# Kernel optimization log

Hardware: AMD Instinct MI355X
Metric: run time of the kernel (lower is better)

Reference implementation:

```python
import jax, jax.numpy as jnp
import numpy as np
from jax.scipy.special import logsumexp

B, N, D, H = 8, 2048, 3, 256
BLUR = 0.001            # geomloss blur
EPS0 = 32.0             # ~diameter^2/2 for unit-std gaussian clouds
N_ITERS = 14            # eps-scaling steps down to blur^2
EPS_LIST = np.geomspace(EPS0, BLUR ** 2, N_ITERS).astype(np.float32)


def _sqdist(x, y):
    # x: [B,N,3], y: [B,M,3] -> [B,N,M] squared euclidean distance
    x2 = jnp.sum(x * x, -1)[:, :, None]
    y2 = jnp.sum(y * y, -1)[:, None, :]
    xy = jnp.einsum('bnd,bmd->bnm', x, y)
    return jnp.maximum(x2 + y2 - 2.0 * xy, 0.0)


def sinkhorn_potential_g(x, y):
    """Log-domain Sinkhorn (p=2 cost ||x-y||^2/2, uniform weights) with
    epsilon scaling; returns second dual potential g over y. Mimics
    geomloss.SamplesLoss('sinkhorn', p=2, blur=0.001, potentials=True)."""
    C = 0.5 * _sqdist(x, y)                      # [B,N,M]
    n, m = x.shape[1], y.shape[1]
    loga = -jnp.log(jnp.float32(n))
    logb = -jnp.log(jnp.float32(m))
    f = jnp.zeros((x.shape[0], n), C.dtype)
    g = jnp.zeros((x.shape[0], m), C.dtype)
    for eps in EPS_LIST:
        f = -eps * logsumexp(logb + (g[:, None, :] - C) / eps, axis=2)
        g = -eps * logsumexp(loga + (f[:, :, None] - C) / eps, axis=1)
    return g


def get_hard_assignment(x, y):
    # idx such that y[idx] is the OT match for x
    g = sinkhorn_potential_g(x, y)                       # [B,M]
    C_minus_g = _sqdist(x, y) - g[:, None, :]            # [B,N,M]
    return jnp.argmin(C_minus_g, axis=2)                 # [B,N]


def setup_inputs() -> dict:
    key = jax.random.key(0)
    ks = jax.random.split(key, 8)
    return {
        'cloud': jax.random.normal(ks[0], (B, N, D), jnp.float32),
        'noise': jax.random.normal(ks[1], (B, N, D), jnp.float32),
        't': jax.random.uniform(ks[2], (B,), jnp.float32),
        'W1': jax.random.normal(ks[3], (D, H), jnp.float32) * 0.1,
        'Wt': jax.random.normal(ks[4], (H,), jnp.float32) * 0.1,
        'b1': jnp.zeros((H,), jnp.float32),
        'W2': jax.random.normal(ks[5], (H, D), jnp.float32) * 0.1,
        'b2': jnp.zeros((D,), jnp.float32),
    }


def reference(cloud, noise, t, W1, Wt, b1, W2, b2):
    # std normalization (torch.std -> unbiased, ddof=1), done under no_grad
    std = jnp.std(cloud, axis=(1, 2), keepdims=True, ddof=1)
    x0 = cloud / std
    idx = get_hard_assignment(noise, x0)                 # [B,N] int
    x0_aligned = jnp.take_along_axis(x0, idx[:, :, None], axis=1)  # [B,N,3]
    tv = t[:, None, None]
    x_t = (1.0 - tv) * x0_aligned + tv * noise
    # stand-in diffusion network: per-point MLP conditioned on t
    h = jax.nn.relu(jnp.einsum('bnd,dh->bnh', x_t, W1) + tv * Wt + b1)
    v_pred = jnp.einsum('bnh,hd->bnd', h, W2) + b2
    v = noise - x0_aligned
    return v_pred, v
```

## Files before the change

### kernel.cpp

```cpp
#include <hip/hip_runtime.h>
#include <math.h>

#define B_ 8
#define N_ 2048
#define D_ 3
#define H_ 256
#define ND_ (N_*D_)
#define BN_ (B_*N_)

__global__ __launch_bounds__(256) void stdprep_kernel(const float* __restrict__ cloud,
    const float* __restrict__ noise,
    float4* __restrict__ x0p, float4* __restrict__ np4,
    float* __restrict__ f, float* __restrict__ g) {
  __shared__ float red[256];
  int b = blockIdx.x, tid = threadIdx.x;
  const float* p = cloud + (size_t)b * ND_;
  float s = 0.f;
  for (int i = tid; i < ND_; i += 256) s += p[i];
  red[tid] = s; __syncthreads();
  for (int off = 128; off > 0; off >>= 1) {
    if (tid < off) red[tid] += red[tid + off];
    __syncthreads();
  }
  float mean = red[0] / (float)ND_;
  __syncthreads();
  float ss = 0.f;
  for (int i = tid; i < ND_; i += 256) { float d = p[i] - mean; ss += d * d; }
  red[tid] = ss; __syncthreads();
  for (int off = 128; off > 0; off >>= 1) {
    if (tid < off) red[tid] += red[tid + off];
    __syncthreads();
  }
  float sd = sqrtf(red[0] / (float)(ND_ - 1));
  int base = b * N_;
  for (int i = tid; i < N_; i += 256) {
    int gi = base + i;
    float cx = cloud[3*gi] / sd, cy = cloud[3*gi+1] / sd, cz = cloud[3*gi+2] / sd;
    x0p[gi] = make_float4(cx, cy, cz, cx*cx + cy*cy + cz*cz);
    float ax = noise[3*gi], ay = noise[3*gi+1], az = noise[3*gi+2];
    np4[gi] = make_float4(ax, ay, az, ax*ax + ay*ay + az*az);
    f[gi] = 0.f; g[gi] = 0.f;
  }
}

__global__ __launch_bounds__(512, 4) void lse_kernel(
    const float4* __restrict__ outer, const float4* __restrict__ inner,
    const float* __restrict__ pin, float* __restrict__ pout,
    float scl, float kk, float hh, float c1, float c2) {
  __shared__ float4 sP[N_];
  int tid = threadIdx.x;
  int b = blockIdx.x & 7;
  int rowBase = (blockIdx.x >> 3) << 4;
  int base = b * N_;
  for (int j = tid; j < N_; j += 512) {
    float4 p = inner[base + j];
    float q = kk * pin[base + j] - hh * p.w;
    sP[j] = make_float4(scl * p.x, scl * p.y, scl * p.z, q);
  }
  __syncthreads();
  int wave = tid >> 6, lane = tid & 63;
  int r0 = base + rowBase + (wave << 1);
  float4 A0 = outer[r0], A1 = outer[r0+1];
  float a0x = scl*A0.x, a0y = scl*A0.y, a0z = scl*A0.z, rc0 = -hh*A0.w;
  float a1x = scl*A1.x, a1y = scl*A1.y, a1z = scl*A1.z, rc1 = -hh*A1.w;
  float v0[32], v1[32];
  float m0 = -INFINITY, m1 = -INFINITY;
#pragma unroll
  for (int jj = 0; jj < 32; ++jj) {
    float4 p = sP[(jj << 6) + lane];
    float t0 = fmaf(p.x, a0x, p.w); t0 = fmaf(p.y, a0y, t0); t0 = fmaf(p.z, a0z, t0);
    v0[jj] = t0; m0 = fmaxf(m0, t0);
    float t1 = fmaf(p.x, a1x, p.w); t1 = fmaf(p.y, a1y, t1); t1 = fmaf(p.z, a1z, t1);
    v1[jj] = t1; m1 = fmaxf(m1, t1);
  }
#pragma unroll
  for (int off = 32; off >= 1; off >>= 1) {
    m0 = fmaxf(m0, __shfl_xor(m0, off, 64));
    m1 = fmaxf(m1, __shfl_xor(m1, off, 64));
  }
  float s0 = 0.f, s1 = 0.f;
#pragma unroll
  for (int jj = 0; jj < 32; ++jj) {
    s0 += __builtin_amdgcn_exp2f(v0[jj] - m0);
    s1 += __builtin_amdgcn_exp2f(v1[jj] - m1);
  }
#pragma unroll
  for (int off = 32; off >= 1; off >>= 1) {
    s0 += __shfl_xor(s0, off, 64);
    s1 += __shfl_xor(s1, off, 64);
  }
  if (lane == 0) {
    pout[r0]   = fmaf(c1, rc0 + m0 + __builtin_amdgcn_logf(s0), c2);
    pout[r0+1] = fmaf(c1, rc1 + m1 + __builtin_amdgcn_logf(s1), c2);
  }
}

__global__ __launch_bounds__(256) void assign_mlp_kernel(
    const float4* __restrict__ np4, const float4* __restrict__ x0p,
    const float* __restrict__ g, const float* __restrict__ t,
    const float* __restrict__ W1, const float* __restrict__ Wt,
    const float* __restrict__ b1, const float* __restrict__ W2,
    const float* __restrict__ b2, float* __restrict__ out) {
  __shared__ float4 sPts[N_];
  __shared__ float  sg[N_];
  __shared__ float  sW1[3*H_], sWt[H_], sb1[H_], sW2[H_*3], sb2[3];
  int tid = threadIdx.x;
  int b = blockIdx.x & 7;
  int rowBase = (blockIdx.x >> 3) << 4;
  int base = b * N_;
  for (int j = tid; j < N_; j += 256) { sPts[j] = x0p[base+j]; sg[j] = g[base+j]; }
  for (int i = tid; i < 3*H_; i += 256) { sW1[i] = W1[i]; sW2[i] = W2[i]; }
  if (tid < H_) { sWt[tid] = Wt[tid]; sb1[tid] = b1[tid]; }
  if (tid < 3) sb2[tid] = b2[tid];
  __syncthreads();
  int wave = tid >> 6, lane = tid & 63;
  int r0 = base + rowBase + (wave << 2);
  float4 A0 = np4[r0], A1 = np4[r0+1], A2 = np4[r0+2], A3 = np4[r0+3];
  float b0 = INFINITY, b1v = INFINITY, b2v = INFINITY, b3v = INFINITY;
  int i0 = 0, i1 = 0, i2 = 0, i3 = 0;
#pragma unroll
  for (int jj = 0; jj < 32; ++jj) {
    int j = (jj << 6) + lane;
    float4 p = sPts[j];
    float gj = sg[j];
    float d0 = A0.x*p.x + A0.y*p.y + A0.z*p.z;
    float v0 = fmaxf(A0.w + p.w - 2.0f*d0, 0.0f) - gj;
    if (v0 < b0) { b0 = v0; i0 = j; }
    float d1 = A1.x*p.x + A1.y*p.y + A1.z*p.z;
    float v1 = fmaxf(A1.w + p.w - 2.0f*d1, 0.0f) - gj;
    if (v1 < b1v) { b1v = v1; i1 = j; }
    float d2 = A2.x*p.x + A2.y*p.y + A2.z*p.z;
    float v2 = fmaxf(A2.w + p.w - 2.0f*d2, 0.0f) - gj;
    if (v2 < b2v) { b2v = v2; i2 = j; }
    float d3 = A3.x*p.x + A3.y*p.y + A3.z*p.z;
    float v3 = fmaxf(A3.w + p.w - 2.0f*d3, 0.0f) - gj;
    if (v3 < b3v) { b3v = v3; i3 = j; }
  }
#pragma unroll
  for (int off = 32; off >= 1; off >>= 1) {
    float ov; int oi;
    ov = __shfl_xor(b0, off, 64);  oi = __shfl_xor(i0, off, 64);
    if (ov < b0 || (ov == b0 && oi < i0)) { b0 = ov; i0 = oi; }
    ov = __shfl_xor(b1v, off, 64); oi = __shfl_xor(i1, off, 64);
    if (ov < b1v || (ov == b1v && oi < i1)) { b1v = ov; i1 = oi; }
    ov = __shfl_xor(b2v, off, 64); oi = __shfl_xor(i2, off, 64);
    if (ov < b2v || (ov == b2v && oi < i2)) { b2v = ov; i2 = oi; }
    ov = __shfl_xor(b3v, off, 64); oi = __shfl_xor(i3, off, 64);
    if (ov < b3v || (ov == b3v && oi < i3)) { b3v = ov; i3 = oi; }
  }
  float tb = t[b];
  int idx[4] = {i0, i1, i2, i3};
  float4 Ar[4] = {A0, A1, A2, A3};
#pragma unroll
  for (int rr = 0; rr < 4; ++rr) {
    float4 A = Ar[rr];
    float4 xa = sPts[idx[rr]];
    float xtx = (1.0f - tb)*xa.x + tb*A.x;
    float xty = (1.0f - tb)*xa.y + tb*A.y;
    float xtz = (1.0f - tb)*xa.z + tb*A.z;
    float acc0 = 0.f, acc1 = 0.f, acc2 = 0.f;
#pragma unroll
    for (int hh = 0; hh < 4; ++hh) {
      int h = (hh << 6) + lane;
      float hv = xtx*sW1[h] + xty*sW1[H_+h] + xtz*sW1[2*H_+h] + tb*sWt[h] + sb1[h];
      hv = fmaxf(hv, 0.0f);
      acc0 += hv * sW2[3*h];
      acc1 += hv * sW2[3*h+1];
      acc2 += hv * sW2[3*h+2];
    }
#pragma unroll
    for (int off = 32; off >= 1; off >>= 1) {
      acc0 += __shfl_xor(acc0, off, 64);
      acc1 += __shfl_xor(acc1, off, 64);
      acc2 += __shfl_xor(acc2, off, 64);
    }
    if (lane == 0) {
      int gi = r0 + rr;
      out[3*gi]   = acc0 + sb2[0];
      out[3*gi+1] = acc1 + sb2[1];
      out[3*gi+2] = acc2 + sb2[2];
      out[3*BN_ + 3*gi]   = A.x - xa.x;
      out[3*BN_ + 3*gi+1] = A.y - xa.y;
      out[3*BN_ + 3*gi+2] = A.z - xa.z;
    }
  }
}

extern "C" void kernel_launch(void* const* d_in, const int* in_sizes, int n_in,
                              void* d_out, int out_size, void* d_ws, size_t ws_size,
                              hipStream_t stream) {
  (void)in_sizes; (void)n_in; (void)out_size; (void)ws_size;
  const float* cloud = (const float*)d_in[0];
  const float* noise = (const float*)d_in[1];
  const float* t     = (const float*)d_in[2];
  const float* W1    = (const float*)d_in[3];
  const float* Wt    = (const float*)d_in[4];
  const float* b1    = (const float*)d_in[5];
  const float* W2    = (const float*)d_in[6];
  const float* b2w   = (const float*)d_in[7];
  float* out = (float*)d_out;

  float* ws   = (float*)d_ws;
  float4* x0p = (float4*)(ws + 16);
  float4* np4 = (float4*)(ws + 16 + 4*BN_);
  float* f    = ws + 16 + 8*BN_;
  float* g    = f + BN_;

  stdprep_kernel<<<B_, 256, 0, stream>>>(cloud, noise, x0p, np4, f, g);

  const double LOG2E = 1.4426950408889634074;
  const double LN2   = 0.6931471805599453094;
  const double logw  = -log(2048.0);
  const double l0 = log10(32.0), l1 = log10(1e-6);
  for (int kit = 0; kit < 14; ++kit) {
    double epsd = pow(10.0, l0 + (l1 - l0) * ((double)kit / 13.0));
    float eps = (float)epsd;
    float kk  = (float)(LOG2E / (double)eps);
    float hh  = 0.5f * kk;
    float scl = sqrtf(kk);
    float c1  = (float)(-(double)eps * LN2);
    float c2  = (float)(-(double)eps * logw);
    lse_kernel<<<B_*(N_/16), 512, 0, stream>>>(np4, x0p, g, f, scl, kk, hh, c1, c2);
    lse_kernel<<<B_*(N_/16), 512, 0, stream>>>(x0p, np4, f, g, scl, kk, hh, c1, c2);
  }

  assign_mlp_kernel<<<B_*(N_/16), 256, 0, stream>>>(np4, x0p, g, t, W1, Wt, b1, W2, b2w, out);
}
```

Baseline: 389.0 us.

## Use online one-pass logsumexp with four rows per wave in Sinkhorn LSE

Replaces the two-pass max-then-sum log-sum-exp with an online running max/sum that rescales the accumulator as it goes. This removes the per-thread value arrays, so the launch bound is raised for higher occupancy. Each wave now processes four rows instead of two, halving the block count and the shared-memory staging per row, and outer-row loads are hoisted before the barrier. The trade-off is roughly twice as many exp2 evaluations per element plus a more complex cross-lane merge, which may hurt an exp-bound kernel.

```diff
diff --git a/kernel.cpp b/kernel.cpp
--- a/kernel.cpp
+++ b/kernel.cpp
@@ -43,55 +43,75 @@
   }
 }
 
-__global__ __launch_bounds__(512, 4) void lse_kernel(
+__global__ __launch_bounds__(512, 8) void lse_kernel(
     const float4* __restrict__ outer, const float4* __restrict__ inner,
     const float* __restrict__ pin, float* __restrict__ pout,
     float scl, float kk, float hh, float c1, float c2) {
   __shared__ float4 sP[N_];
   int tid = threadIdx.x;
   int b = blockIdx.x & 7;
-  int rowBase = (blockIdx.x >> 3) << 4;
+  int rowBase = (blockIdx.x >> 3) << 5;
   int base = b * N_;
+  int wave = tid >> 6, lane = tid & 63;
+  int r0 = base + rowBase + (wave << 2);
+  float4 A0 = outer[r0], A1 = outer[r0+1], A2 = outer[r0+2], A3 = outer[r0+3];
   for (int j = tid; j < N_; j += 512) {
     float4 p = inner[base + j];
     float q = kk * pin[base + j] - hh * p.w;
     sP[j] = make_float4(scl * p.x, scl * p.y, scl * p.z, q);
   }
-  __syncthreads();
-  int wave = tid >> 6, lane = tid & 63;
-  int r0 = base + rowBase + (wave << 1);
-  float4 A0 = outer[r0], A1 = outer[r0+1];
   float a0x = scl*A0.x, a0y = scl*A0.y, a0z = scl*A0.z, rc0 = -hh*A0.w;
   float a1x = scl*A1.x, a1y = scl*A1.y, a1z = scl*A1.z, rc1 = -hh*A1.w;
-  float v0[32], v1[32];
-  float m0 = -INFINITY, m1 = -INFINITY;
+  float a2x = scl*A2.x, a2y = scl*A2.y, a2z = scl*A2.z, rc2 = -hh*A2.w;
+  float a3x = scl*A3.x, a3y = scl*A3.y, a3z = scl*A3.z, rc3 = -hh*A3.w;
+  __syncthreads();
+  float m0 = -INFINITY, m1 = -INFINITY, m2 = -INFINITY, m3 = -INFINITY;
+  float s0 = 0.f, s1 = 0.f, s2 = 0.f, s3 = 0.f;
 #pragma unroll
   for (int jj = 0; jj < 32; ++jj) {
     float4 p = sP[(jj << 6) + lane];
     float t0 = fmaf(p.x, a0x, p.w); t0 = fmaf(p.y, a0y, t0); t0 = fmaf(p.z, a0z, t0);
-    v0[jj] = t0; m0 = fmaxf(m0, t0);
+    float n0 = fmaxf(m0, t0);
+    s0 = fmaf(s0, __builtin_amdgcn_exp2f(m0 - n0), __builtin_amdgcn_exp2f(t0 - n0));
+    m0 = n0;
     float t1 = fmaf(p.x, a1x, p.w); t1 = fmaf(p.y, a1y, t1); t1 = fmaf(p.z, a1z, t1);
-    v1[jj] = t1; m1 = fmaxf(m1, t1);
+    float n1 = fmaxf(m1, t1);
+    s1 = fmaf(s1, __builtin_amdgcn_exp2f(m1 - n1), __builtin_amdgcn_exp2f(t1 - n1));
+    m1 = n1;
+    float t2 = fmaf(p.x, a2x, p.w); t2 = fmaf(p.y, a2y, t2); t2 = fmaf(p.z, a2z, t2);
+    float n2 = fmaxf(m2, t2);
+    s2 = fmaf(s2, __builtin_amdgcn_exp2f(m2 - n2), __builtin_amdgcn_exp2f(t2 - n2));
+    m2 = n2;
+    float t3 = fmaf(p.x, a3x, p.w); t3 = fmaf(p.y, a3y, t3); t3 = fmaf(p.z, a3z, t3);
+    float n3 = fmaxf(m3, t3);
+    s3 = fmaf(s3, __builtin_amdgcn_exp2f(m3 - n3), __builtin_amdgcn_exp2f(t3 - n3));
+    m3 = n3;
   }
 #pragma unroll
   for (int off = 32; off >= 1; off >>= 1) {
-    m0 = fmaxf(m0, __shfl_xor(m0, off, 64));
-    m1 = fmaxf(m1, __shfl_xor(m1, off, 64));
-  }
-  float s0 = 0.f, s1 = 0.f;
-#pragma unroll
-  for (int jj = 0; jj < 32; ++jj) {
-    s0 += __builtin_amdgcn_exp2f(v0[jj] - m0);
-    s1 += __builtin_amdgcn_exp2f(v1[jj] - m1);
-  }
-#pragma unroll
-  for (int off = 32; off >= 1; off >>= 1) {
-    s0 += __shfl_xor(s0, off, 64);
-    s1 += __shfl_xor(s1, off, 64);
+    float mo, so, nn;
+    mo = __shfl_xor(m0, off, 64); so = __shfl_xor(s0, off, 64);
+    nn = fmaxf(m0, mo);
+    s0 = fmaf(s0, __builtin_amdgcn_exp2f(m0 - nn), so * __builtin_amdgcn_exp2f(mo - nn));
+    m0 = nn;
+    mo = __shfl_xor(m1, off, 64); so = __shfl_xor(s1, off, 64);
+    nn = fmaxf(m1, mo);
+    s1 = fmaf(s1, __builtin_amdgcn_exp2f(m1 - nn), so * __builtin_amdgcn_exp2f(mo - nn));
+    m1 = nn;
+    mo = __shfl_xor(m2, off, 64); so = __shfl_xor(s2, off, 64);
+    nn = fmaxf(m2, mo);
+    s2 = fmaf(s2, __builtin_amdgcn_exp2f(m2 - nn), so * __builtin_amdgcn_exp2f(mo - nn));
+    m2 = nn;
+    mo = __shfl_xor(m3, off, 64); so = __shfl_xor(s3, off, 64);
+    nn = fmaxf(m3, mo);
+    s3 = fmaf(s3, __builtin_amdgcn_exp2f(m3 - nn), so * __builtin_amdgcn_exp2f(mo - nn));
+    m3 = nn;
   }
   if (lane == 0) {
     pout[r0]   = fmaf(c1, rc0 + m0 + __builtin_amdgcn_logf(s0), c2);
     pout[r0+1] = fmaf(c1, rc1 + m1 + __builtin_amdgcn_logf(s1), c2);
+    pout[r0+2] = fmaf(c1, rc2 + m2 + __builtin_amdgcn_logf(s2), c2);
+    pout[r0+3] = fmaf(c1, rc3 + m3 + __builtin_amdgcn_logf(s3), c2);
   }
 }
 
@@ -220,8 +240,8 @@
     float scl = sqrtf(kk);
     float c1  = (float)(-(double)eps * LN2);
     float c2  = (float)(-(double)eps * logw);
-    lse_kernel<<<B_*(N_/16), 512, 0, stream>>>(np4, x0p, g, f, scl, kk, hh, c1, c2);
-    lse_kernel<<<B_*(N_/16), 512, 0, stream>>>(x0p, np4, f, g, scl, kk, hh, c1, c2);
+    lse_kernel<<<B_*(N_/32), 512, 0, stream>>>(np4, x0p, g, f, scl, kk, hh, c1, c2);
+    lse_kernel<<<B_*(N_/32), 512, 0, stream>>>(x0p, np4, f, g, scl, kk, hh, c1, c2);
   }
 
   assign_mlp_kernel<<<B_*(N_/16), 256, 0, stream>>>(np4, x0p, g, t, W1, Wt, b1, W2, b2w, out);
```

Result: slower. 513.3 us (+31.9%).

## Process four rows per wave in LSE kernel with chunked online logsumexp

Applied to the files above, without the earlier changes.

Each wave now handles four rows instead of two, so each block covers 32 rows and the grid is halved. This halves the redundant shared-memory staging of the inner point set per block, and each LDS read is reused across more rows. To keep register pressure bounded, the 2048 columns are processed in two chunks of 16 values per lane, merged with an online max/sum rescaling, and the wave reduction merges (max, sum) pairs together. The outer-row loads are hoisted above the barrier. The trade-off is extra exp2 calls for rescaling and a grid of only 512 blocks, which lowers occupancy and parallelism.

```diff
diff --git a/kernel.cpp b/kernel.cpp
--- a/kernel.cpp
+++ b/kernel.cpp
@@ -50,48 +50,87 @@
   __shared__ float4 sP[N_];
   int tid = threadIdx.x;
   int b = blockIdx.x & 7;
-  int rowBase = (blockIdx.x >> 3) << 4;
+  int rowBase = (blockIdx.x >> 3) << 5;
   int base = b * N_;
+  int wave = tid >> 6, lane = tid & 63;
+  int r0 = base + rowBase + (wave << 2);
+  float4 A0 = outer[r0], A1 = outer[r0+1], A2 = outer[r0+2], A3 = outer[r0+3];
   for (int j = tid; j < N_; j += 512) {
     float4 p = inner[base + j];
     float q = kk * pin[base + j] - hh * p.w;
     sP[j] = make_float4(scl * p.x, scl * p.y, scl * p.z, q);
   }
-  __syncthreads();
-  int wave = tid >> 6, lane = tid & 63;
-  int r0 = base + rowBase + (wave << 1);
-  float4 A0 = outer[r0], A1 = outer[r0+1];
   float a0x = scl*A0.x, a0y = scl*A0.y, a0z = scl*A0.z, rc0 = -hh*A0.w;
   float a1x = scl*A1.x, a1y = scl*A1.y, a1z = scl*A1.z, rc1 = -hh*A1.w;
-  float v0[32], v1[32];
-  float m0 = -INFINITY, m1 = -INFINITY;
-#pragma unroll
-  for (int jj = 0; jj < 32; ++jj) {
-    float4 p = sP[(jj << 6) + lane];
-    float t0 = fmaf(p.x, a0x, p.w); t0 = fmaf(p.y, a0y, t0); t0 = fmaf(p.z, a0z, t0);
-    v0[jj] = t0; m0 = fmaxf(m0, t0);
-    float t1 = fmaf(p.x, a1x, p.w); t1 = fmaf(p.y, a1y, t1); t1 = fmaf(p.z, a1z, t1);
-    v1[jj] = t1; m1 = fmaxf(m1, t1);
+  float a2x = scl*A2.x, a2y = scl*A2.y, a2z = scl*A2.z, rc2 = -hh*A2.w;
+  float a3x = scl*A3.x, a3y = scl*A3.y, a3z = scl*A3.z, rc3 = -hh*A3.w;
+  __syncthreads();
+  float M0 = -INFINITY, M1 = -INFINITY, M2 = -INFINITY, M3 = -INFINITY;
+  float S0 = 0.f, S1 = 0.f, S2 = 0.f, S3 = 0.f;
+#pragma unroll
+  for (int c = 0; c < 2; ++c) {
+    float v0[16], v1[16], v2[16], v3[16];
+    float m0 = -INFINITY, m1 = -INFINITY, m2 = -INFINITY, m3 = -INFINITY;
+#pragma unroll
+    for (int jj = 0; jj < 16; ++jj) {
+      float4 p = sP[(((c << 4) + jj) << 6) + lane];
+      float t0 = fmaf(p.x, a0x, p.w); t0 = fmaf(p.y, a0y, t0); t0 = fmaf(p.z, a0z, t0);
+      v0[jj] = t0; m0 = fmaxf(m0, t0);
+      float t1 = fmaf(p.x, a1x, p.w); t1 = fmaf(p.y, a1y, t1); t1 = fmaf(p.z, a1z, t1);
+      v1[jj] = t1; m1 = fmaxf(m1, t1);
+      float t2 = fmaf(p.x, a2x, p.w); t2 = fmaf(p.y, a2y, t2); t2 = fmaf(p.z, a2z, t2);
+      v2[jj] = t2; m2 = fmaxf(m2, t2);
+      float t3 = fmaf(p.x, a3x, p.w); t3 = fmaf(p.y, a3y, t3); t3 = fmaf(p.z, a3z, t3);
+      v3[jj] = t3; m3 = fmaxf(m3, t3);
+    }
+    asm volatile("" ::: "memory");
+    float s0 = 0.f, s1 = 0.f, s2 = 0.f, s3 = 0.f;
+#pragma unroll
+    for (int jj = 0; jj < 16; ++jj) {
+      s0 += __builtin_amdgcn_exp2f(v0[jj] - m0);
+      s1 += __builtin_amdgcn_exp2f(v1[jj] - m1);
+      s2 += __builtin_amdgcn_exp2f(v2[jj] - m2);
+      s3 += __builtin_amdgcn_exp2f(v3[jj] - m3);
+    }
+    float n;
+    n = fmaxf(M0, m0);
+    S0 = fmaf(S0, __builtin_amdgcn_exp2f(M0 - n), s0 * __builtin_amdgcn_exp2f(m0 - n));
+    M0 = n;
+    n = fmaxf(M1, m1);
+    S1 = fmaf(S1, __builtin_amdgcn_exp2f(M1 - n), s1 * __builtin_amdgcn_exp2f(m1 - n));
+    M1 = n;
+    n = fmaxf(M2, m2);
+    S2 = fmaf(S2, __builtin_amdgcn_exp2f(M2 - n), s2 * __builtin_amdgcn_exp2f(m2 - n));
+    M2 = n;
+    n = fmaxf(M3, m3);
+    S3 = fmaf(S3, __builtin_amdgcn_exp2f(M3 - n), s3 * __builtin_amdgcn_exp2f(m3 - n));
+    M3 = n;
   }
 #pragma unroll
   for (int off = 32; off >= 1; off >>= 1) {
-    m0 = fmaxf(m0, __shfl_xor(m0, off, 64));
-    m1 = fmaxf(m1, __shfl_xor(m1, off, 64));
-  }
-  float s0 = 0.f, s1 = 0.f;
-#pragma unroll
-  for (int jj = 0; jj < 32; ++jj) {
-    s0 += __builtin_amdgcn_exp2f(v0[jj] - m0);
-    s1 += __builtin_amdgcn_exp2f(v1[jj] - m1);
-  }
-#pragma unroll
-  for (int off = 32; off >= 1; off >>= 1) {
-    s0 += __shfl_xor(s0, off, 64);
-    s1 += __shfl_xor(s1, off, 64);
+    float mo, so, nn;
+    mo = __shfl_xor(M0, off, 64); so = __shfl_xor(S0, off, 64);
+    nn = fmaxf(M0, mo);
+    S0 = fmaf(S0, __builtin_amdgcn_exp2f(M0 - nn), so * __builtin_amdgcn_exp2f(mo - nn));
+    M0 = nn;
+    mo = __shfl_xor(M1, off, 64); so = __shfl_xor(S1, off, 64);
+    nn = fmaxf(M1, mo);
+    S1 = fmaf(S1, __builtin_amdgcn_exp2f(M1 - nn), so * __builtin_amdgcn_exp2f(mo - nn));
+    M1 = nn;
+    mo = __shfl_xor(M2, off, 64); so = __shfl_xor(S2, off, 64);
+    nn = fmaxf(M2, mo);
+    S2 = fmaf(S2, __builtin_amdgcn_exp2f(M2 - nn), so * __builtin_amdgcn_exp2f(mo - nn));
+    M2 = nn;
+    mo = __shfl_xor(M3, off, 64); so = __shfl_xor(S3, off, 64);
+    nn = fmaxf(M3, mo);
+    S3 = fmaf(S3, __builtin_amdgcn_exp2f(M3 - nn), so * __builtin_amdgcn_exp2f(mo - nn));
+    M3 = nn;
   }
   if (lane == 0) {
-    pout[r0]   = fmaf(c1, rc0 + m0 + __builtin_amdgcn_logf(s0), c2);
-    pout[r0+1] = fmaf(c1, rc1 + m1 + __builtin_amdgcn_logf(s1), c2);
+    pout[r0]   = fmaf(c1, rc0 + M0 + __builtin_amdgcn_logf(S0), c2);
+    pout[r0+1] = fmaf(c1, rc1 + M1 + __builtin_amdgcn_logf(S1), c2);
+    pout[r0+2] = fmaf(c1, rc2 + M2 + __builtin_amdgcn_logf(S2), c2);
+    pout[r0+3] = fmaf(c1, rc3 + M3 + __builtin_amdgcn_logf(S3), c2);
   }
 }
 
@@ -220,8 +259,8 @@
     float scl = sqrtf(kk);
     float c1  = (float)(-(double)eps * LN2);
     float c2  = (float)(-(double)eps * logw);
-    lse_kernel<<<B_*(N_/16), 512, 0, stream>>>(np4, x0p, g, f, scl, kk, hh, c1, c2);
-    lse_kernel<<<B_*(N_/16), 512, 0, stream>>>(x0p, np4, f, g, scl, kk, hh, c1, c2);
+    lse_kernel<<<B_*(N_/32), 512, 0, stream>>>(np4, x0p, g, f, scl, kk, hh, c1, c2);
+    lse_kernel<<<B_*(N_/32), 512, 0, stream>>>(x0p, np4, f, g, scl, kk, hh, c1, c2);
   }
 
   assign_mlp_kernel<<<B_*(N_/16), 256, 0, stream>>>(np4, x0p, g, t, W1, Wt, b1, W2, b2w, out);
```

New measurement: 426.2 us. 9.6% more time.
